# Kernel tuning notes

Measured on AMD Instinct MI355X. Metric: run time of the kernel, lower is better.

The kernel has to match this reference:

```python
import jax, jax.numpy as jnp
import numpy as np

M = 0.4        # margin
H = 0.333      # margin scaler slope
S = 64.0       # logit scale
BN_MEAN = 20.0     # running_mean of norm normalizer (affine=False, eval stats)
BN_VAR = 100.0 * 100.0
BN_EPS = 1e-3


def setup_inputs() -> dict:
    key = jax.random.key(0)
    k1, k2, k3 = jax.random.split(key, 3)
    embs = jax.random.normal(k1, (1024, 512), dtype=jnp.float32)
    weight = jax.random.normal(k2, (100000, 512), dtype=jnp.float32)
    labels = jax.random.randint(k3, (1024,), 0, 100000)
    return {"embs": embs, "weight": weight, "labels": labels}


def reference(embs, weight, labels):
    n = embs.shape[0]
    rows = jnp.arange(n)
    # feature norms and cosine logits
    norms = jnp.linalg.norm(embs, axis=1, keepdims=True)            # [N,1]
    w_norm = weight / jnp.linalg.norm(weight, axis=1, keepdims=True)  # [C,D]
    logits = (embs / norms) @ w_norm.T                               # [N,C]
    # norm-adaptive margin scaler (BatchNorm1d with running stats, affine=False)
    g = (norms[:, 0] - BN_MEAN) / jnp.sqrt(BN_VAR + BN_EPS)
    g = jnp.clip(g * H, -1.0, 1.0)                                   # [N]
    # angular margin at the label position
    theta = jnp.arccos(jnp.clip(logits.astype(jnp.float32), -0.999, 0.999))
    theta = theta.at[rows, labels].add(-M * g)
    logits_m = jnp.cos(jnp.clip(theta, 0.0, jnp.pi))
    # additive margin at the label position
    logits_m = logits_m.at[rows, labels].add(-(1.0 + M) * g)
    # scaled softmax cross-entropy (mean over batch)
    logp = jax.nn.log_softmax(logits_m * S, axis=-1)
    return -jnp.mean(logp[rows, labels])
```

## Files before the change

### kernel.cpp

```cpp
#include <hip/hip_runtime.h>
#include <math.h>

constexpr int N_ROWS = 1024;
constexpr int DDIM   = 512;
constexpr int C_CLS  = 100000;
constexpr float MARG = 0.4f;
constexpr int WPAD   = 100352;
constexpr int NT2    = 392;
constexpr int NT_FB  = 782;
constexpr int TSLOT  = 256 * 32;

typedef __attribute__((ext_vector_type(8))) short bf16x8;
typedef __attribute__((ext_vector_type(4))) float f32x4;
typedef __attribute__((address_space(1))) const void gvoid_t;
typedef __attribute__((address_space(3))) void lvoid_t;

__device__ __forceinline__ unsigned int f2bf(float x) {
    union { float f; unsigned int u; } v; v.f = x;
    return (v.u + 0x7FFFu + ((v.u >> 16) & 1u)) >> 16;
}

__device__ __forceinline__ float wave_sum(float s) {
    #pragma unroll
    for (int m = 1; m < 64; m <<= 1) s += __shfl_xor(s, m, 64);
    return s;
}

__global__ __launch_bounds__(256) void prep_embs(const float* __restrict__ embs,
                                                 float* __restrict__ g,
                                                 unsigned short* __restrict__ ehat) {
    const int row  = blockIdx.x * 4 + (threadIdx.x >> 6);
    const int lane = threadIdx.x & 63;
    const float4* src = (const float4*)(embs + (size_t)row * DDIM + lane * 8);
    const float4 a = src[0], b = src[1];
    float ss = a.x*a.x + a.y*a.y + a.z*a.z + a.w*a.w
             + b.x*b.x + b.y*b.y + b.z*b.z + b.w*b.w;
    ss = wave_sum(ss);
    const float norm = sqrtf(ss);
    const float rn = 1.f / norm;
    if (lane == 0) {
        float gg = (norm - 20.f) / sqrtf(10000.f + 1e-3f) * 0.333f;
        gg = fminf(fmaxf(gg, -1.f), 1.f);
        g[row] = gg;
    }
    uint4 pk;
    pk.x = f2bf(a.x*rn) | (f2bf(a.y*rn) << 16);
    pk.y = f2bf(a.z*rn) | (f2bf(a.w*rn) << 16);
    pk.z = f2bf(b.x*rn) | (f2bf(b.y*rn) << 16);
    pk.w = f2bf(b.z*rn) | (f2bf(b.w*rn) << 16);
    *(uint4*)(ehat + (size_t)row * DDIM + lane * 8) = pk;
}

__global__ __launch_bounds__(256) void prep_what(const float* __restrict__ w,
                                                 unsigned short* __restrict__ what) {
    const int row  = blockIdx.x * 4 + (threadIdx.x >> 6);
    const int lane = threadIdx.x & 63;
    const float4* src = (const float4*)(w + (size_t)row * DDIM + lane * 8);
    const float4 a = src[0], b = src[1];
    float ss = a.x*a.x + a.y*a.y + a.z*a.z + a.w*a.w
             + b.x*b.x + b.y*b.y + b.z*b.z + b.w*b.w;
    ss = wave_sum(ss);
    const float rn = rsqrtf(ss);
    uint4 pk;
    pk.x = f2bf(a.x*rn) | (f2bf(a.y*rn) << 16);
    pk.y = f2bf(a.z*rn) | (f2bf(a.w*rn) << 16);
    pk.z = f2bf(b.x*rn) | (f2bf(b.y*rn) << 16);
    pk.w = f2bf(b.z*rn) | (f2bf(b.w*rn) << 16);
    *(uint4*)(what + (size_t)row * DDIM + lane * 8) = pk;
}

__global__ __launch_bounds__(256) void prep_wnorm(const float* __restrict__ w,
                                                  float* __restrict__ rnormw) {
    const int row  = blockIdx.x * 4 + (threadIdx.x >> 6);
    const int lane = threadIdx.x & 63;
    const float4* src = (const float4*)(w + (size_t)row * DDIM + lane * 8);
    const float4 a = src[0], b = src[1];
    float ss = a.x*a.x + a.y*a.y + a.z*a.z + a.w*a.w
             + b.x*b.x + b.y*b.y + b.z*b.z + b.w*b.w;
    ss = wave_sum(ss);
    if (lane == 0) rnormw[row] = 1.f / sqrtf(ss);
}

__device__ __forceinline__ void stage_tile(const unsigned short* __restrict__ src,
                                           int grow0, unsigned short* tile,
                                           int kbase, int tid, int wv) {
    #pragma unroll
    for (int i = 0; i < 2; ++i) {
        const int r  = i * 128 + (tid >> 2);
        const int lc = (tid & 3) ^ ((r >> 1) & 3);
        const unsigned short* g = src + (size_t)(grow0 + r) * DDIM + kbase + lc * 8;
        __builtin_amdgcn_global_load_lds((gvoid_t*)g,
            (lvoid_t*)(tile + i * 4096 + wv * 512), 16, 0, 0);
    }
}
__device__ __forceinline__ bf16x8 frag32(const unsigned short* tile, int row, int lane) {
    const int pc = (lane >> 4) ^ ((row >> 1) & 3);
    return *(const bf16x8*)(tile + row * 32 + pc * 8);
}

__global__ __launch_bounds__(512, 2) void gemm256p(
        const unsigned short* __restrict__ ehat,
        const unsigned short* __restrict__ what,
        const int* __restrict__ labels,
        float* __restrict__ psum,
        float* __restrict__ dlab)
{
    __shared__ __align__(16) unsigned short Abuf[4 * TSLOT];
    __shared__ __align__(16) unsigned short Bbuf[4 * TSLOT];

    const int tid  = threadIdx.x;
    const int lane = tid & 63;
    const int wv   = tid >> 6;
    const int wr   = wv >> 2;
    const int wc   = wv & 3;

    const int nchunk = (int)gridDim.x >> 3;
    const int wgid   = ((int)blockIdx.x & 7) * nchunk + ((int)blockIdx.x >> 3);
    const int tile_c = wgid >> 2;
    const int tile_r = wgid & 3;
    const int row0   = tile_r * 256;
    const int col0   = tile_c * 256;

    f32x4 acc[8][4];
    #pragma unroll
    for (int m = 0; m < 8; ++m)
        #pragma unroll
        for (int n = 0; n < 4; ++n) acc[m][n] = f32x4{0.f, 0.f, 0.f, 0.f};

    #pragma unroll
    for (int t = 0; t < 3; ++t) {
        stage_tile(ehat, row0, Abuf + t * TSLOT, t * 32, tid, wv);
        stage_tile(what, col0, Bbuf + t * TSLOT, t * 32, tid, wv);
    }
    asm volatile("s_waitcnt vmcnt(8)" ::: "memory");
    __builtin_amdgcn_s_barrier();

    auto body = [&](int h, bool do_stage) {
        if (do_stage) {
            const int hn = h + 3;
            stage_tile(ehat, row0, Abuf + (hn & 3) * TSLOT, hn * 32, tid, wv);
            stage_tile(what, col0, Bbuf + (hn & 3) * TSLOT, hn * 32, tid, wv);
        }
        const unsigned short* At = Abuf + (h & 3) * TSLOT;
        const unsigned short* Bt = Bbuf + (h & 3) * TSLOT;
        bf16x8 af[8], bf[4];
        #pragma unroll
        for (int m = 0; m < 8; ++m)
            af[m] = frag32(At, wr * 128 + m * 16 + (lane & 15), lane);
        #pragma unroll
        for (int n = 0; n < 4; ++n)
            bf[n] = frag32(Bt, wc * 64 + n * 16 + (lane & 15), lane);
        __builtin_amdgcn_s_setprio(1);
        #pragma unroll
        for (int m = 0; m < 8; ++m)
            #pragma unroll
            for (int n = 0; n < 4; ++n)
                acc[m][n] = __builtin_amdgcn_mfma_f32_16x16x32_bf16(af[m], bf[n], acc[m][n], 0, 0, 0);
        __builtin_amdgcn_s_setprio(0);
    };

    for (int h = 0; h < 13; ++h) {
        body(h, true);
        asm volatile("s_waitcnt vmcnt(8)" ::: "memory");
        __builtin_amdgcn_s_barrier();
    }
    body(13, false);
    asm volatile("s_waitcnt vmcnt(4)" ::: "memory");
    __builtin_amdgcn_s_barrier();
    body(14, false);
    asm volatile("s_waitcnt vmcnt(0)" ::: "memory");
    __builtin_amdgcn_s_barrier();
    body(15, false);

    float* red = (float*)&Abuf[0];
    #pragma unroll
    for (int m = 0; m < 8; ++m) {
        #pragma unroll
        for (int j = 0; j < 4; ++j) {
            const int lrow  = wr * 128 + m * 16 + ((lane >> 4) << 2) + j;
            const int r_abs = row0 + lrow;
            const int lab   = labels[r_abs];
            float s = 0.f;
            #pragma unroll
            for (int n = 0; n < 4; ++n) {
                const int c_abs = col0 + wc * 64 + n * 16 + (lane & 15);
                float v = acc[m][n][j];
                v = fminf(fmaxf(v, -0.999f), 0.999f);
                if (c_abs == lab) dlab[r_abs] = v;
                if (c_abs < C_CLS) s += __expf(64.f * v - 64.f);
            }
            #pragma unroll
            for (int msk = 1; msk < 16; msk <<= 1) s += __shfl_xor(s, msk, 64);
            if ((lane & 15) == 0) red[wc * 256 + lrow] = s;
        }
    }
    __syncthreads();
    for (int t = tid; t < 256; t += 512)
        psum[(size_t)(row0 + t) * NT2 + tile_c] = red[t] + red[256 + t] + red[512 + t] + red[768 + t];
}

__global__ __launch_bounds__(256, 2) void gemm_fused_fb(
        const unsigned short* __restrict__ ehat,
        const float* __restrict__ weight,
        const float* __restrict__ rnormw,
        const int* __restrict__ labels,
        float* __restrict__ psum,
        float* __restrict__ dlab)
{
    constexpr int BM = 128, BN = 128, BK = 32;
    __shared__ __align__(16) unsigned short Asf[BM * BK];
    __shared__ __align__(16) unsigned short Bsf[BN * BK];
    __shared__ float redbuf[2][BM];

    const int bid    = blockIdx.x;
    const int tile_c = bid >> 3;
    const int tile_r = bid & 7;
    const int row0   = tile_r * BM;
    const int col0   = tile_c * BN;

    const int tid  = threadIdx.x;
    const int lane = tid & 63;
    const int wv   = tid >> 6;
    const int wr   = wv >> 1;
    const int wc   = wv & 1;

    f32x4 acc[4][4];
    #pragma unroll
    for (int m = 0; m < 4; ++m)
        #pragma unroll
        for (int n = 0; n < 4; ++n) acc[m][n] = f32x4{0.f, 0.f, 0.f, 0.f};

    const int kq    = tid & 7;
    const int brow0 = tid >> 3;
    int   cidx[4];
    float rnv[4];
    #pragma unroll
    for (int p = 0; p < 4; ++p) {
        int c = col0 + p * 32 + brow0;
        c = c < C_CLS ? c : C_CLS - 1;
        cidx[p] = c;
        rnv[p]  = rnormw[c];
    }

    for (int kt = 0; kt < DDIM / BK; ++kt) {
        const int kbase = kt * BK;
        #pragma unroll
        for (int call = 0; call < 2; ++call) {
            const int chunk = call * 256 + tid;
            const uint4 d = *(const uint4*)(ehat + (size_t)(row0 + (chunk >> 2)) * DDIM
                                            + kbase + (chunk & 3) * 8);
            *(uint4*)(Asf + chunk * 8) = d;
        }
        #pragma unroll
        for (int p = 0; p < 4; ++p) {
            const float4 wd = *(const float4*)(weight + (size_t)cidx[p] * DDIM + kbase + kq * 4);
            const float r = rnv[p];
            const unsigned int lo = f2bf(wd.x * r) | (f2bf(wd.y * r) << 16);
            const unsigned int hi = f2bf(wd.z * r) | (f2bf(wd.w * r) << 16);
            *(uint2*)(Bsf + (p * 32 + brow0) * BK + kq * 4) = make_uint2(lo, hi);
        }
        __syncthreads();
        bf16x8 af[4], bfr[4];
        const int lr  = lane & 15;
        const int lko = (lane >> 4) * 8;
        #pragma unroll
        for (int m = 0; m < 4; ++m)
            af[m] = *(const bf16x8*)(Asf + (wr * 64 + m * 16 + lr) * BK + lko);
        #pragma unroll
        for (int n = 0; n < 4; ++n)
            bfr[n] = *(const bf16x8*)(Bsf + (wc * 64 + n * 16 + lr) * BK + lko);
        #pragma unroll
        for (int m = 0; m < 4; ++m)
            #pragma unroll
            for (int n = 0; n < 4; ++n)
                acc[m][n] = __builtin_amdgcn_mfma_f32_16x16x32_bf16(af[m], bfr[n], acc[m][n], 0, 0, 0);
        __syncthreads();
    }

    #pragma unroll
    for (int m = 0; m < 4; ++m) {
        #pragma unroll
        for (int j = 0; j < 4; ++j) {
            const int lrow  = wr * 64 + m * 16 + ((lane >> 4) << 2) + j;
            const int r_abs = row0 + lrow;
            const int lab   = labels[r_abs];
            float s = 0.f;
            #pragma unroll
            for (int n = 0; n < 4; ++n) {
                const int c_abs = col0 + wc * 64 + n * 16 + (lane & 15);
                float v = acc[m][n][j];
                v = fminf(fmaxf(v, -0.999f), 0.999f);
                if (c_abs == lab) dlab[r_abs] = v;
                if (c_abs < C_CLS) s += __expf(64.f * v - 64.f);
            }
            #pragma unroll
            for (int msk = 1; msk < 16; msk <<= 1) s += __shfl_xor(s, msk, 64);
            if ((lane & 15) == 0) redbuf[wc][lrow] = s;
        }
    }
    __syncthreads();
    for (int t = tid; t < BM; t += 256)
        psum[(size_t)(row0 + t) * NT_FB + tile_c] = redbuf[0][t] + redbuf[1][t];
}

__global__ __launch_bounds__(256) void reduce_rows(const float* __restrict__ psum,
                                                   const float* __restrict__ dlab,
                                                   const float* __restrict__ g,
                                                   float* __restrict__ losses, int nt) {
    const int row  = blockIdx.x * 4 + (threadIdx.x >> 6);
    const int lane = threadIdx.x & 63;
    const float* p = psum + (size_t)row * nt;
    float s = 0.f;
    for (int t = lane; t < nt; t += 64) s += p[t];
    s = wave_sum(s);
    if (lane == 0) {
        const float v  = dlab[row];
        const float gg = g[row];
        float th = acosf(v) - MARG * gg;
        th = fminf(fmaxf(th, 0.f), 3.14159265358979323846f);
        const float vm = cosf(th) - (1.f + MARG) * gg;
        s = s - __expf(64.f * v - 64.f) + __expf(64.f * vm - 64.f);
        losses[row] = 64.f + logf(s) - 64.f * vm;
    }
}

__global__ __launch_bounds__(256) void final_mean(const float* __restrict__ losses,
                                                  float* __restrict__ out) {
    const int tid = threadIdx.x;
    float s = 0.f;
    #pragma unroll
    for (int i = 0; i < 4; ++i) s += losses[tid + i * 256];
    s = wave_sum(s);
    __shared__ float red[4];
    if ((tid & 63) == 0) red[tid >> 6] = s;
    __syncthreads();
    if (tid == 0) out[0] = (red[0] + red[1] + red[2] + red[3]) * (1.f / 1024.f);
}

extern "C" void kernel_launch(void* const* d_in, const int* in_sizes, int n_in,
                              void* d_out, int out_size, void* d_ws, size_t ws_size,
                              hipStream_t stream) {
    const float* embs   = (const float*)d_in[0];
    const float* weight = (const float*)d_in[1];
    const int*   labels = (const int*)d_in[2];
    float* out = (float*)d_out;
    float* ws  = (float*)d_ws;

    const size_t WHAT_F = (size_t)WPAD * DDIM / 2;
    const size_t EHAT_F = (size_t)N_ROWS * DDIM / 2;
    const size_t PSUM_F = (size_t)N_ROWS * NT2;
    const size_t NEED_F = WHAT_F + EHAT_F + PSUM_F + 3 * 1024;

    if (ws_size >= NEED_F * sizeof(float)) {
        unsigned short* what = (unsigned short*)ws;
        unsigned short* ehat = (unsigned short*)(ws + WHAT_F);
        float* psum   = ws + WHAT_F + EHAT_F;
        float* gbuf   = psum + PSUM_F;
        float* dlab   = gbuf + 1024;
        float* losses = dlab + 1024;

        prep_embs<<<N_ROWS / 4, 256, 0, stream>>>(embs, gbuf, ehat);
        prep_what<<<C_CLS / 4, 256, 0, stream>>>(weight, what);
        gemm256p<<<NT2 * 4, 512, 0, stream>>>(ehat, what, labels, psum, dlab);
        reduce_rows<<<N_ROWS / 4, 256, 0, stream>>>(psum, dlab, gbuf, losses, NT2);
        final_mean<<<1, 256, 0, stream>>>(losses, out);
    } else {
        float* rnormw = ws + 0;
        float* gbuf   = ws + 100352;
        float* dlab   = ws + 101376;
        float* losses = ws + 102400;
        unsigned short* ehat = (unsigned short*)(ws + 103424);
        float* psum   = ws + 103424 + 262144;

        prep_embs <<<N_ROWS / 4, 256, 0, stream>>>(embs, gbuf, ehat);
        prep_wnorm<<<C_CLS / 4, 256, 0, stream>>>(weight, rnormw);
        gemm_fused_fb<<<NT_FB * 8, 256, 0, stream>>>(ehat, weight, rnormw, labels, psum, dlab);
        reduce_rows<<<N_ROWS / 4, 256, 0, stream>>>(psum, dlab, gbuf, losses, NT_FB);
        final_mean<<<1, 256, 0, stream>>>(losses, out);
    }
}
```

Before: 222.6 us.

## Switch main GEMM path to FP8 e4m3 MFMA with 128x128 tiles

Normalized embeddings and weights are now quantized to FP8 e4m3 instead of bf16, and the main GEMM uses the scaled 16x16x128 f8f6f4 MFMA with 128x128 tiles and double-buffered 128-wide K stages. This halves the bytes written and read for the normalized weight matrix and doubles matrix throughput per instruction. The cost is far lower precision in the cosine logits, which are multiplied by 64 before the softmax, so the loss may drift beyond tolerance. More tiles also means twice as many partial-sum columns for the row reduction.

```diff
diff --git a/kernel.cpp b/kernel.cpp
--- a/kernel.cpp
+++ b/kernel.cpp
@@ -5,15 +5,18 @@
 constexpr int DDIM   = 512;
 constexpr int C_CLS  = 100000;
 constexpr float MARG = 0.4f;
-constexpr int WPAD   = 100352;
-constexpr int NT2    = 392;
+constexpr int NT8    = 784;
+constexpr int WPAD8  = 100352;
 constexpr int NT_FB  = 782;
-constexpr int TSLOT  = 256 * 32;
 
 typedef __attribute__((ext_vector_type(8))) short bf16x8;
 typedef __attribute__((ext_vector_type(4))) float f32x4;
+typedef __attribute__((ext_vector_type(4))) int   i32x4;
+typedef __attribute__((ext_vector_type(8))) int   i32x8;
 typedef __attribute__((address_space(1))) const void gvoid_t;
 typedef __attribute__((address_space(3))) void lvoid_t;
+
+#define WAITV(N) asm volatile("s_waitcnt vmcnt(" #N ")" ::: "memory")
 
 __device__ __forceinline__ unsigned int f2bf(float x) {
     union { float f; unsigned int u; } v; v.f = x;
@@ -24,6 +27,188 @@
     #pragma unroll
     for (int m = 1; m < 64; m <<= 1) s += __shfl_xor(s, m, 64);
     return s;
+}
+
+#if __has_builtin(__builtin_amdgcn_cvt_pk_fp8_f32)
+__device__ __forceinline__ unsigned int pk4_e4m3(float a, float b, float c, float d) {
+    unsigned int u = (unsigned int)__builtin_amdgcn_cvt_pk_fp8_f32(a, b, 0, false);
+    u = (unsigned int)__builtin_amdgcn_cvt_pk_fp8_f32(c, d, (int)u, true);
+    return u;
+}
+#else
+__device__ __forceinline__ unsigned int sw_e4m3(float x) {
+    x = fminf(fmaxf(x, -448.f), 448.f);
+    unsigned int s = (x < 0.f) ? 0x80u : 0u;
+    float ax = fabsf(x);
+    if (ax < 7.8125e-3f) {
+        int q = (int)rintf(ax * 512.f);
+        if (q >= 8) return s | 0x08;
+        return s | (unsigned int)q;
+    }
+    int e; float m = frexpf(ax, &e);
+    int q = (int)rintf(m * 16.f);
+    if (q == 16) { q = 8; e += 1; }
+    int E = e - 1 + 7;
+    if (E > 15) { E = 15; q = 14; }
+    return s | ((unsigned int)E << 3) | (unsigned int)(q - 8);
+}
+__device__ __forceinline__ unsigned int pk4_e4m3(float a, float b, float c, float d) {
+    return sw_e4m3(a) | (sw_e4m3(b) << 8) | (sw_e4m3(c) << 16) | (sw_e4m3(d) << 24);
+}
+#endif
+
+__global__ __launch_bounds__(256) void prep_embs8(const float* __restrict__ embs,
+                                                  float* __restrict__ g,
+                                                  unsigned char* __restrict__ ehat8) {
+    const int row  = blockIdx.x * 4 + (threadIdx.x >> 6);
+    const int lane = threadIdx.x & 63;
+    const float4* src = (const float4*)(embs + (size_t)row * DDIM + lane * 8);
+    const float4 a = src[0], b = src[1];
+    float ss = a.x*a.x + a.y*a.y + a.z*a.z + a.w*a.w
+             + b.x*b.x + b.y*b.y + b.z*b.z + b.w*b.w;
+    ss = wave_sum(ss);
+    const float norm = sqrtf(ss);
+    const float rn = 1.f / norm;
+    if (lane == 0) {
+        float gg = (norm - 20.f) / sqrtf(10000.f + 1e-3f) * 0.333f;
+        gg = fminf(fmaxf(gg, -1.f), 1.f);
+        g[row] = gg;
+    }
+    uint2 pk;
+    pk.x = pk4_e4m3(a.x*rn, a.y*rn, a.z*rn, a.w*rn);
+    pk.y = pk4_e4m3(b.x*rn, b.y*rn, b.z*rn, b.w*rn);
+    *(uint2*)(ehat8 + (size_t)row * DDIM + lane * 8) = pk;
+}
+
+__global__ __launch_bounds__(256) void prep_what8(const float* __restrict__ w,
+                                                  unsigned char* __restrict__ what8) {
+    const int row  = blockIdx.x * 4 + (threadIdx.x >> 6);
+    const int lane = threadIdx.x & 63;
+    const float4* src = (const float4*)(w + (size_t)row * DDIM + lane * 8);
+    const float4 a = src[0], b = src[1];
+    float ss = a.x*a.x + a.y*a.y + a.z*a.z + a.w*a.w
+             + b.x*b.x + b.y*b.y + b.z*b.z + b.w*b.w;
+    ss = wave_sum(ss);
+    const float rn = rsqrtf(ss);
+    uint2 pk;
+    pk.x = pk4_e4m3(a.x*rn, a.y*rn, a.z*rn, a.w*rn);
+    pk.y = pk4_e4m3(b.x*rn, b.y*rn, b.z*rn, b.w*rn);
+    *(uint2*)(what8 + (size_t)row * DDIM + lane * 8) = pk;
+}
+
+__device__ __forceinline__ void stage8(const unsigned char* __restrict__ src, int grow0,
+                                       unsigned char* tile, int kbase, int wv, int lane) {
+    const int lr = lane >> 3;
+    const int lc = (lane & 7) ^ lr;
+    #pragma unroll
+    for (int i = 0; i < 4; ++i) {
+        const int s = wv * 4 + i;
+        const unsigned char* gp = src + (size_t)(grow0 + s * 8 + lr) * DDIM + kbase + lc * 16;
+        __builtin_amdgcn_global_load_lds((gvoid_t*)gp, (lvoid_t*)(tile + s * 1024), 16, 0, 0);
+    }
+}
+__device__ __forceinline__ i32x8 frag8(const unsigned char* tile, int row, int lane) {
+    const int c0 = ((lane >> 4) * 2 + 0) ^ (row & 7);
+    const int c1 = ((lane >> 4) * 2 + 1) ^ (row & 7);
+    const i32x4 lo = *(const i32x4*)(tile + row * 128 + c0 * 16);
+    const i32x4 hi = *(const i32x4*)(tile + row * 128 + c1 * 16);
+    i32x8 r;
+    r[0] = lo[0]; r[1] = lo[1]; r[2] = lo[2]; r[3] = lo[3];
+    r[4] = hi[0]; r[5] = hi[1]; r[6] = hi[2]; r[7] = hi[3];
+    return r;
+}
+
+__global__ __launch_bounds__(256, 2) void gemm128f8(
+        const unsigned char* __restrict__ ehat8,
+        const unsigned char* __restrict__ what8,
+        const int* __restrict__ labels,
+        float* __restrict__ psum,
+        float* __restrict__ dlab)
+{
+    __shared__ __align__(16) unsigned char Ab[2][128 * 128];
+    __shared__ __align__(16) unsigned char Bb[2][128 * 128];
+    __shared__ float redbuf[2][128];
+
+    const int tid  = threadIdx.x;
+    const int lane = tid & 63;
+    const int wv   = tid >> 6;
+    const int wr   = wv >> 1;
+    const int wc   = wv & 1;
+
+    const int wgid   = ((int)blockIdx.x & 7) * 784 + ((int)blockIdx.x >> 3);
+    const int tile_c = wgid >> 3;
+    const int tile_r = wgid & 7;
+    const int row0   = tile_r * 128;
+    const int col0   = tile_c * 128;
+
+    f32x4 acc[4][4];
+    #pragma unroll
+    for (int m = 0; m < 4; ++m)
+        #pragma unroll
+        for (int n = 0; n < 4; ++n) acc[m][n] = f32x4{0.f, 0.f, 0.f, 0.f};
+
+    stage8(ehat8, row0, Ab[0], 0,   wv, lane);
+    stage8(what8, col0, Bb[0], 0,   wv, lane);
+    stage8(ehat8, row0, Ab[1], 128, wv, lane);
+    stage8(what8, col0, Bb[1], 128, wv, lane);
+    WAITV(8);
+    __builtin_amdgcn_s_barrier();
+
+    #pragma unroll
+    for (int t = 0; t < 4; ++t) {
+        const unsigned char* At = Ab[t & 1];
+        const unsigned char* Bt = Bb[t & 1];
+        i32x8 aF[4], bF[4];
+        #pragma unroll
+        for (int m = 0; m < 4; ++m)
+            aF[m] = frag8(At, wr * 64 + m * 16 + (lane & 15), lane);
+        #pragma unroll
+        for (int n = 0; n < 4; ++n)
+            bF[n] = frag8(Bt, wc * 64 + n * 16 + (lane & 15), lane);
+        asm volatile("s_waitcnt lgkmcnt(0)" ::: "memory");
+        __builtin_amdgcn_sched_barrier(0);
+        __builtin_amdgcn_s_barrier();
+        if (t < 2) {
+            stage8(ehat8, row0, Ab[t & 1], (t + 2) * 128, wv, lane);
+            stage8(what8, col0, Bb[t & 1], (t + 2) * 128, wv, lane);
+        }
+        __builtin_amdgcn_s_setprio(1);
+        #pragma unroll
+        for (int m = 0; m < 4; ++m)
+            #pragma unroll
+            for (int n = 0; n < 4; ++n)
+                acc[m][n] = __builtin_amdgcn_mfma_scale_f32_16x16x128_f8f6f4(
+                                aF[m], bF[n], acc[m][n], 0, 0, 0, 127, 0, 127);
+        __builtin_amdgcn_s_setprio(0);
+        if (t < 2)      { WAITV(8); }
+        else if (t == 2){ WAITV(0); }
+        if (t < 3) __builtin_amdgcn_s_barrier();
+    }
+
+    #pragma unroll
+    for (int m = 0; m < 4; ++m) {
+        #pragma unroll
+        for (int j = 0; j < 4; ++j) {
+            const int lrow  = wr * 64 + m * 16 + ((lane >> 4) << 2) + j;
+            const int r_abs = row0 + lrow;
+            const int lab   = labels[r_abs];
+            float s = 0.f;
+            #pragma unroll
+            for (int n = 0; n < 4; ++n) {
+                const int c_abs = col0 + wc * 64 + n * 16 + (lane & 15);
+                float v = acc[m][n][j];
+                v = fminf(fmaxf(v, -0.999f), 0.999f);
+                if (c_abs == lab) dlab[r_abs] = v;
+                if (c_abs < C_CLS) s += __expf(64.f * v - 64.f);
+            }
+            #pragma unroll
+            for (int msk = 1; msk < 16; msk <<= 1) s += __shfl_xor(s, msk, 64);
+            if ((lane & 15) == 0) redbuf[wc][lrow] = s;
+        }
+    }
+    __syncthreads();
+    for (int t = tid; t < 128; t += 256)
+        psum[(size_t)(row0 + t) * NT8 + tile_c] = redbuf[0][t] + redbuf[1][t];
 }
 
 __global__ __launch_bounds__(256) void prep_embs(const float* __restrict__ embs,
@@ -51,24 +236,6 @@
     *(uint4*)(ehat + (size_t)row * DDIM + lane * 8) = pk;
 }
 
-__global__ __launch_bounds__(256) void prep_what(const float* __restrict__ w,
-                                                 unsigned short* __restrict__ what) {
-    const int row  = blockIdx.x * 4 + (threadIdx.x >> 6);
-    const int lane = threadIdx.x & 63;
-    const float4* src = (const float4*)(w + (size_t)row * DDIM + lane * 8);
-    const float4 a = src[0], b = src[1];
-    float ss = a.x*a.x + a.y*a.y + a.z*a.z + a.w*a.w
-             + b.x*b.x + b.y*b.y + b.z*b.z + b.w*b.w;
-    ss = wave_sum(ss);
-    const float rn = rsqrtf(ss);
-    uint4 pk;
-    pk.x = f2bf(a.x*rn) | (f2bf(a.y*rn) << 16);
-    pk.y = f2bf(a.z*rn) | (f2bf(a.w*rn) << 16);
-    pk.z = f2bf(b.x*rn) | (f2bf(b.y*rn) << 16);
-    pk.w = f2bf(b.z*rn) | (f2bf(b.w*rn) << 16);
-    *(uint4*)(what + (size_t)row * DDIM + lane * 8) = pk;
-}
-
 __global__ __launch_bounds__(256) void prep_wnorm(const float* __restrict__ w,
                                                   float* __restrict__ rnormw) {
     const int row  = blockIdx.x * 4 + (threadIdx.x >> 6);
@@ -79,124 +246,6 @@
              + b.x*b.x + b.y*b.y + b.z*b.z + b.w*b.w;
     ss = wave_sum(ss);
     if (lane == 0) rnormw[row] = 1.f / sqrtf(ss);
-}
-
-__device__ __forceinline__ void stage_tile(const unsigned short* __restrict__ src,
-                                           int grow0, unsigned short* tile,
-                                           int kbase, int tid, int wv) {
-    #pragma unroll
-    for (int i = 0; i < 2; ++i) {
-        const int r  = i * 128 + (tid >> 2);
-        const int lc = (tid & 3) ^ ((r >> 1) & 3);
-        const unsigned short* g = src + (size_t)(grow0 + r) * DDIM + kbase + lc * 8;
-        __builtin_amdgcn_global_load_lds((gvoid_t*)g,
-            (lvoid_t*)(tile + i * 4096 + wv * 512), 16, 0, 0);
-    }
-}
-__device__ __forceinline__ bf16x8 frag32(const unsigned short* tile, int row, int lane) {
-    const int pc = (lane >> 4) ^ ((row >> 1) & 3);
-    return *(const bf16x8*)(tile + row * 32 + pc * 8);
-}
-
-__global__ __launch_bounds__(512, 2) void gemm256p(
-        const unsigned short* __restrict__ ehat,
-        const unsigned short* __restrict__ what,
-        const int* __restrict__ labels,
-        float* __restrict__ psum,
-        float* __restrict__ dlab)
-{
-    __shared__ __align__(16) unsigned short Abuf[4 * TSLOT];
-    __shared__ __align__(16) unsigned short Bbuf[4 * TSLOT];
-
-    const int tid  = threadIdx.x;
-    const int lane = tid & 63;
-    const int wv   = tid >> 6;
-    const int wr   = wv >> 2;
-    const int wc   = wv & 3;
-
-    const int nchunk = (int)gridDim.x >> 3;
-    const int wgid   = ((int)blockIdx.x & 7) * nchunk + ((int)blockIdx.x >> 3);
-    const int tile_c = wgid >> 2;
-    const int tile_r = wgid & 3;
-    const int row0   = tile_r * 256;
-    const int col0   = tile_c * 256;
-
-    f32x4 acc[8][4];
-    #pragma unroll
-    for (int m = 0; m < 8; ++m)
-        #pragma unroll
-        for (int n = 0; n < 4; ++n) acc[m][n] = f32x4{0.f, 0.f, 0.f, 0.f};
-
-    #pragma unroll
-    for (int t = 0; t < 3; ++t) {
-        stage_tile(ehat, row0, Abuf + t * TSLOT, t * 32, tid, wv);
-        stage_tile(what, col0, Bbuf + t * TSLOT, t * 32, tid, wv);
-    }
-    asm volatile("s_waitcnt vmcnt(8)" ::: "memory");
-    __builtin_amdgcn_s_barrier();
-
-    auto body = [&](int h, bool do_stage) {
-        if (do_stage) {
-            const int hn = h + 3;
-            stage_tile(ehat, row0, Abuf + (hn & 3) * TSLOT, hn * 32, tid, wv);
-            stage_tile(what, col0, Bbuf + (hn & 3) * TSLOT, hn * 32, tid, wv);
-        }
-        const unsigned short* At = Abuf + (h & 3) * TSLOT;
-        const unsigned short* Bt = Bbuf + (h & 3) * TSLOT;
-        bf16x8 af[8], bf[4];
-        #pragma unroll
-        for (int m = 0; m < 8; ++m)
-            af[m] = frag32(At, wr * 128 + m * 16 + (lane & 15), lane);
-        #pragma unroll
-        for (int n = 0; n < 4; ++n)
-            bf[n] = frag32(Bt, wc * 64 + n * 16 + (lane & 15), lane);
-        __builtin_amdgcn_s_setprio(1);
-        #pragma unroll
-        for (int m = 0; m < 8; ++m)
-            #pragma unroll
-            for (int n = 0; n < 4; ++n)
-                acc[m][n] = __builtin_amdgcn_mfma_f32_16x16x32_bf16(af[m], bf[n], acc[m][n], 0, 0, 0);
-        __builtin_amdgcn_s_setprio(0);
-    };
-
-    for (int h = 0; h < 13; ++h) {
-        body(h, true);
-        asm volatile("s_waitcnt vmcnt(8)" ::: "memory");
-        __builtin_amdgcn_s_barrier();
-    }
-    body(13, false);
-    asm volatile("s_waitcnt vmcnt(4)" ::: "memory");
-    __builtin_amdgcn_s_barrier();
-    body(14, false);
-    asm volatile("s_waitcnt vmcnt(0)" ::: "memory");
-    __builtin_amdgcn_s_barrier();
-    body(15, false);
-
-    float* red = (float*)&Abuf[0];
-    #pragma unroll
-    for (int m = 0; m < 8; ++m) {
-        #pragma unroll
-        for (int j = 0; j < 4; ++j) {
-            const int lrow  = wr * 128 + m * 16 + ((lane >> 4) << 2) + j;
-            const int r_abs = row0 + lrow;
-            const int lab   = labels[r_abs];
-            float s = 0.f;
-            #pragma unroll
-            for (int n = 0; n < 4; ++n) {
-                const int c_abs = col0 + wc * 64 + n * 16 + (lane & 15);
-                float v = acc[m][n][j];
-                v = fminf(fmaxf(v, -0.999f), 0.999f);
-                if (c_abs == lab) dlab[r_abs] = v;
-                if (c_abs < C_CLS) s += __expf(64.f * v - 64.f);
-            }
-            #pragma unroll
-            for (int msk = 1; msk < 16; msk <<= 1) s += __shfl_xor(s, msk, 64);
-            if ((lane & 15) == 0) red[wc * 256 + lrow] = s;
-        }
-    }
-    __syncthreads();
-    for (int t = tid; t < 256; t += 512)
-        psum[(size_t)(row0 + t) * NT2 + tile_c] = red[t] + red[256 + t] + red[512 + t] + red[768 + t];
 }
 
 __global__ __launch_bounds__(256, 2) void gemm_fused_fb(
@@ -344,27 +393,28 @@
     const float* weight = (const float*)d_in[1];
     const int*   labels = (const int*)d_in[2];
     float* out = (float*)d_out;
-    float* ws  = (float*)d_ws;
-
-    const size_t WHAT_F = (size_t)WPAD * DDIM / 2;
-    const size_t EHAT_F = (size_t)N_ROWS * DDIM / 2;
-    const size_t PSUM_F = (size_t)N_ROWS * NT2;
-    const size_t NEED_F = WHAT_F + EHAT_F + PSUM_F + 3 * 1024;
-
-    if (ws_size >= NEED_F * sizeof(float)) {
-        unsigned short* what = (unsigned short*)ws;
-        unsigned short* ehat = (unsigned short*)(ws + WHAT_F);
-        float* psum   = ws + WHAT_F + EHAT_F;
-        float* gbuf   = psum + PSUM_F;
+    unsigned char* wsb = (unsigned char*)d_ws;
+
+    const size_t WHAT8_B = (size_t)WPAD8 * DDIM;
+    const size_t EHAT8_B = (size_t)N_ROWS * DDIM;
+    const size_t PSUM_B  = (size_t)N_ROWS * NT8 * 4;
+    const size_t NEED_B  = WHAT8_B + EHAT8_B + PSUM_B + 3 * 4096;
+
+    if (ws_size >= NEED_B) {
+        unsigned char* what8 = wsb;
+        unsigned char* ehat8 = wsb + WHAT8_B;
+        float* psum   = (float*)(wsb + WHAT8_B + EHAT8_B);
+        float* gbuf   = psum + (size_t)N_ROWS * NT8;
         float* dlab   = gbuf + 1024;
         float* losses = dlab + 1024;
 
-        prep_embs<<<N_ROWS / 4, 256, 0, stream>>>(embs, gbuf, ehat);
-        prep_what<<<C_CLS / 4, 256, 0, stream>>>(weight, what);
-        gemm256p<<<NT2 * 4, 512, 0, stream>>>(ehat, what, labels, psum, dlab);
-        reduce_rows<<<N_ROWS / 4, 256, 0, stream>>>(psum, dlab, gbuf, losses, NT2);
+        prep_embs8<<<N_ROWS / 4, 256, 0, stream>>>(embs, gbuf, ehat8);
+        prep_what8<<<C_CLS / 4, 256, 0, stream>>>(weight, what8);
+        gemm128f8<<<NT8 * 8, 256, 0, stream>>>(ehat8, what8, labels, psum, dlab);
+        reduce_rows<<<N_ROWS / 4, 256, 0, stream>>>(psum, dlab, gbuf, losses, NT8);
         final_mean<<<1, 256, 0, stream>>>(losses, out);
     } else {
+        float* ws = (float*)d_ws;
         float* rnormw = ws + 0;
         float* gbuf   = ws + 100352;
         float* dlab   = ws + 101376;
```

Measured after the change: 178.7 us. -19.7%, faster.
